# Optimization experiments

Measured on AMD Instinct MI355X. Metric: run time of the kernel, lower is better.

Reference implementation:

```python
import jax, jax.numpy as jnp
import numpy as np

TOP_K = 8          # n_activated_experts
ROUTE_SCALE = 2.5  # route_scale


def setup_inputs() -> dict:
    key = jax.random.key(0)
    k1, k2, k3 = jax.random.split(key, 3)
    T, D, E = 16384, 7168, 256
    x = jax.random.normal(k1, (T, D), dtype=jnp.float32)
    # nn.Linear weight layout: [out_features, in_features]
    W = jax.random.normal(k2, (E, D), dtype=jnp.float32) * (1.0 / np.sqrt(D))
    bias = jax.random.normal(k3, (E,), dtype=jnp.float32) * 0.01
    return {"x": x, "W": W, "bias": bias}


def reference(x, W, bias):
    # logits: [T, E] = x [T, D] @ W.T [D, E]
    logits = jnp.einsum("td,ed->te", x, W)
    scores = jax.nn.sigmoid(logits)              # original_scores
    biased = scores + bias                       # bias only affects expert selection
    _, indices = jax.lax.top_k(biased, TOP_K)    # [T, K] int32
    weights = jnp.take_along_axis(scores, indices, axis=-1)  # gather unbiased scores
    weights = weights / jnp.sum(weights, axis=-1, keepdims=True)  # sigmoid renorm
    weights = weights * ROUTE_SCALE
    return weights.astype(x.dtype), indices
```

## Files before the change

### kernel.cpp

```cpp
#include <hip/hip_runtime.h>
#include <cmath>

namespace {

typedef _Float16 half8 __attribute__((ext_vector_type(8)));
typedef float f32x4 __attribute__((ext_vector_type(4)));

constexpr int kTokens = 16384;
constexpr int kD      = 7168;
constexpr int kE      = 256;
constexpr int kTopK   = 8;
constexpr float kRouteScale = 2.5f;

constexpr int BM     = 64;
constexpr int BK     = 32;
constexpr int KSTEP  = 128;
constexpr int NT     = kD / BK;
constexpr int NSTEP  = kD / KSTEP;
constexpr float kS  = 4096.0f;
constexpr float kC  = 0.000244140625f;
constexpr size_t kWsTileB = 32768;
constexpr size_t kWsNeed  = (size_t)NT * kWsTileB;

__global__ void wconv_kernel(const float* __restrict__ W, unsigned char* __restrict__ ws)
{
    const int e = blockIdx.x;
    const int t = threadIdx.x;
    const float* src = W + (size_t)e * kD + (size_t)t * 8;
    float v[8];
    *reinterpret_cast<float4*>(v)     = *reinterpret_cast<const float4*>(src);
    *reinterpret_cast<float4*>(v + 4) = *reinterpret_cast<const float4*>(src + 4);
    half8 h, l;
#pragma unroll
    for (int j = 0; j < 8; ++j) {
        _Float16 hh = (_Float16)v[j];
        h[j] = hh;
        l[j] = (_Float16)((v[j] - (float)hh) * kS);
    }
    const int kt = t >> 2;
    const int kg = t & 3;
    const size_t off = (size_t)kt * kWsTileB +
                       (size_t)(((e >> 4) << 6) + (kg << 4) + (e & 15)) * 16;
    *reinterpret_cast<half8*>(ws + off)         = h;
    *reinterpret_cast<half8*>(ws + off + 16384) = l;
}

__global__ __launch_bounds__(1024, 4)
void gate_mfma(const float* __restrict__ x,
               const unsigned char* __restrict__ wst,
               const float* __restrict__ bias,
               float* __restrict__ out)
{
    __shared__ unsigned char lds[65792];

    const int t    = threadIdx.x;
    const int lane = t & 63;
    const int w    = t >> 6;
    const int cg   = w >> 1;
    const int rg   = w & 1;
    const int kk0  = cg & 3;
    const int m0   = blockIdx.x * BM;
    const int l15  = lane & 15;
    const int lg   = lane >> 4;

    const int srow = t >> 4;
    const int skc  = t & 15;
    const unsigned waddr = (unsigned)(((skc >> 2) << 13) + ((srow >> 4) << 10) +
                                      ((skc & 3) << 8) + ((((srow & 15) ^ skc) & 15) << 4));
    const float* xsrc = x + (size_t)(m0 + srow) * kD + (size_t)(skc * 8);

    const unsigned char* wb = wst + (size_t)(cg * 2) * 1024 + (size_t)lane * 16;

    f32x4 acc0[2][2], acc1[2][2], accL[2][2];
#pragma unroll
    for (int i = 0; i < 2; ++i)
#pragma unroll
        for (int j = 0; j < 2; ++j) {
            acc0[i][j] = f32x4{0.f,0.f,0.f,0.f};
            acc1[i][j] = f32x4{0.f,0.f,0.f,0.f};
            accL[i][j] = f32x4{0.f,0.f,0.f,0.f};
        }

    half8 bh[2][2];
    half8 bl[2];

    auto LOADBH = [&](int pp, int kt) {
        const unsigned char* p = wb + (size_t)kt * kWsTileB;
        bh[pp][0] = *reinterpret_cast<const half8*>(p);
        bh[pp][1] = *reinterpret_cast<const half8*>(p + 1024);
    };
    auto LOADBL = [&](int kt) {
        const unsigned char* p = wb + (size_t)kt * kWsTileB + 16384;
        bl[0] = *reinterpret_cast<const half8*>(p);
        bl[1] = *reinterpret_cast<const half8*>(p + 1024);
    };
    auto WRITESTEP = [&](unsigned base, const float4& a, const float4& b) {
        float v[8];
        *reinterpret_cast<float4*>(v)     = a;
        *reinterpret_cast<float4*>(v + 4) = b;
        half8 h0, h1;
#pragma unroll
        for (int j = 0; j < 8; ++j) {
            const _Float16 hh = (_Float16)v[j];
            h0[j] = hh;
            h1[j] = (_Float16)((v[j] - (float)hh) * kS);
        }
        *reinterpret_cast<half8*>(&lds[base + waddr])        = h0;
        *reinterpret_cast<half8*>(&lds[base + waddr + 4096]) = h1;
    };

    {
        float4 a = *reinterpret_cast<const float4*>(xsrc);
        float4 b = *reinterpret_cast<const float4*>(xsrc + 4);
        LOADBH(0, kk0);
        WRITESTEP(0, a, b);
    }
    __syncthreads();

    for (int s = 0; s < NSTEP; ++s) {
        const unsigned bufc = (unsigned)((s & 1) << 15);
        const unsigned bufn = (unsigned)(((s + 1) & 1) << 15);
        const bool pre = (s + 1 < NSTEP);
        float4 nv0{0,0,0,0}, nv1{0,0,0,0};
        if (pre) {
            const float* p = xsrc + (s + 1) * KSTEP;
            nv0 = *reinterpret_cast<const float4*>(p);
            nv1 = *reinterpret_cast<const float4*>(p + 4);
        }

#pragma unroll
        for (int n = 0; n < 4; ++n) {
            const int kk = (kk0 + n) & 3;
            const int kt = s * 4 + kk;
            LOADBL(kt);
            const int kt_next = (n < 3) ? (s * 4 + ((kk0 + n + 1) & 3))
                                        : ((s + 1) * 4 + kk0);
            if (kt_next < NT) LOADBH((n & 1) ^ 1, kt_next);

            half8 xh[2], xm[2];
#pragma unroll
            for (int i = 0; i < 2; ++i) {
                const int rf = rg * 2 + i;
                const unsigned base = bufc + (unsigned)(kk << 13) + (unsigned)(rf << 10) +
                                      (unsigned)(lg << 8) +
                                      (unsigned)((((l15 ^ ((kk << 2) + lg)) & 15) << 4));
                xh[i] = *reinterpret_cast<const half8*>(&lds[base]);
                xm[i] = *reinterpret_cast<const half8*>(&lds[base + 4096]);
            }

            __builtin_amdgcn_s_setprio(1);
#pragma unroll
            for (int i = 0; i < 2; ++i)
#pragma unroll
                for (int j = 0; j < 2; ++j)
                    acc0[i][j] = __builtin_amdgcn_mfma_f32_16x16x32_f16(xh[i], bh[n & 1][j], acc0[i][j], 0, 0, 0);
#pragma unroll
            for (int i = 0; i < 2; ++i)
#pragma unroll
                for (int j = 0; j < 2; ++j)
                    acc1[i][j] = __builtin_amdgcn_mfma_f32_16x16x32_f16(xm[i], bh[n & 1][j], acc1[i][j], 0, 0, 0);
#pragma unroll
            for (int i = 0; i < 2; ++i)
#pragma unroll
                for (int j = 0; j < 2; ++j)
                    acc1[i][j] = __builtin_amdgcn_mfma_f32_16x16x32_f16(xh[i], bl[j], acc1[i][j], 0, 0, 0);
            __builtin_amdgcn_s_setprio(0);
        }

        if (pre) WRITESTEP(bufn, nv0, nv1);

        if (((s + 1) & 7) == 0) {
#pragma unroll
            for (int i = 0; i < 2; ++i)
#pragma unroll
                for (int j = 0; j < 2; ++j) {
                    accL[i][j] += acc0[i][j];
                    acc0[i][j] = f32x4{0.f,0.f,0.f,0.f};
                }
        }
        __syncthreads();
    }

    float (*sc)[257] = reinterpret_cast<float (*)[257]>(lds);
#pragma unroll
    for (int j = 0; j < 2; ++j) {
        const int col  = cg * 32 + j * 16 + l15;
        const float bv = bias[col];
#pragma unroll
        for (int i = 0; i < 2; ++i) {
            f32x4 z = (accL[i][j] + acc0[i][j]) + kC * acc1[i][j];
#pragma unroll
            for (int r = 0; r < 4; ++r) {
                const int row = rg * 32 + i * 16 + lg * 4 + r;
                const float sg = 1.0f / (1.0f + expf(-z[r]));
                sc[row][col] = sg + bv;
            }
        }
    }
    __syncthreads();

    const int rr = t >> 4;
    const int g  = t & 15;

    float cval[kTopK];
    int   cidx[kTopK];

#pragma unroll
    for (int r = 0; r < kTopK; ++r) {
        float best = -INFINITY;
        int   bi   = kE;
        const float* rowp = sc[rr] + g * 16;
#pragma unroll 8
        for (int c = 0; c < 16; ++c) {
            const float v  = rowp[c];
            const int   ci = g * 16 + c;
            if (v > best || (v == best && ci < bi)) { best = v; bi = ci; }
        }
#pragma unroll
        for (int off = 8; off > 0; off >>= 1) {
            const float ov = __shfl_xor(best, off, 16);
            const int   oi = __shfl_xor(bi,   off, 16);
            if (ov > best || (ov == best && oi < bi)) { best = ov; bi = oi; }
        }
        cval[r] = best;
        cidx[r] = bi;
        if ((bi >> 4) == g) sc[rr][bi] = -INFINITY;
    }

    if (g == 0) {
        float uw[kTopK];
        float wsum = 0.0f;
#pragma unroll
        for (int r = 0; r < kTopK; ++r) {
            uw[r] = cval[r] - bias[cidx[r]];
            wsum += uw[r];
        }
        const float scale = kRouteScale / wsum;
        const size_t grow = (size_t)(m0 + rr);
#pragma unroll
        for (int r = 0; r < kTopK; ++r)
            out[grow * kTopK + r] = uw[r] * scale;
#pragma unroll
        for (int r = 0; r < kTopK; ++r)
            out[(size_t)kTokens * kTopK + grow * kTopK + r] = (float)cidx[r];
    }
}

constexpr int FBM = 32;
constexpr int FBK = 32;
constexpr int XS_STRIDE = 36;
constexpr int SC_STRIDE = 260;

__global__ __launch_bounds__(256, 2)
void gate_fused(const float* __restrict__ x,
                const float* __restrict__ W,
                const float* __restrict__ bias,
                float* __restrict__ out)
{
    __shared__ float smem[FBK * XS_STRIDE + FBK * kE];
    float (*xs)[XS_STRIDE] = reinterpret_cast<float (*)[XS_STRIDE]>(smem);
    float (*ws)[kE]        = reinterpret_cast<float (*)[kE]>(smem + FBK * XS_STRIDE);
    float (*sc)[SC_STRIDE] = reinterpret_cast<float (*)[SC_STRIDE]>(smem);

    const int t  = threadIdx.x;
    const int tx = t & 31;
    const int ty = t >> 5;
    const int m0 = blockIdx.x * FBM;
    const int lm = t >> 3;
    const int lc = t & 7;

    float acc[4][8];
    float cmp[4][8];
#pragma unroll
    for (int i = 0; i < 4; ++i)
#pragma unroll
        for (int j = 0; j < 8; ++j) { acc[i][j] = 0.0f; cmp[i][j] = 0.0f; }

    const float* xrow = x + (size_t)(m0 + lm) * kD;
    const float* wrow = W + (size_t)t * kD;

    for (int k0 = 0; k0 < kD; k0 += FBK) {
        float4 xv = *reinterpret_cast<const float4*>(xrow + k0 + 4 * lc);
        float4 wv[8];
#pragma unroll
        for (int i = 0; i < 8; ++i)
            wv[i] = *reinterpret_cast<const float4*>(wrow + k0 + 4 * i);
        __syncthreads();
        xs[4 * lc + 0][lm] = xv.x; xs[4 * lc + 1][lm] = xv.y;
        xs[4 * lc + 2][lm] = xv.z; xs[4 * lc + 3][lm] = xv.w;
#pragma unroll
        for (int i = 0; i < 8; ++i) {
            ws[4 * i + 0][t] = wv[i].x; ws[4 * i + 1][t] = wv[i].y;
            ws[4 * i + 2][t] = wv[i].z; ws[4 * i + 3][t] = wv[i].w;
        }
        __syncthreads();
        float p[4][8];
#pragma unroll
        for (int i = 0; i < 4; ++i)
#pragma unroll
            for (int j = 0; j < 8; ++j) p[i][j] = 0.0f;
#pragma unroll
        for (int k = 0; k < FBK; ++k) {
            float a[4], b[8];
            *reinterpret_cast<float4*>(a)     = *reinterpret_cast<const float4*>(&xs[k][4 * ty]);
            *reinterpret_cast<float4*>(b)     = *reinterpret_cast<const float4*>(&ws[k][4 * tx]);
            *reinterpret_cast<float4*>(b + 4) = *reinterpret_cast<const float4*>(&ws[k][128 + 4 * tx]);
#pragma unroll
            for (int i = 0; i < 4; ++i)
#pragma unroll
                for (int j = 0; j < 8; ++j)
                    p[i][j] = fmaf(a[i], b[j], p[i][j]);
        }
#pragma unroll
        for (int i = 0; i < 4; ++i)
#pragma unroll
            for (int j = 0; j < 8; ++j) {
                const float y = p[i][j] - cmp[i][j];
                const float s = acc[i][j] + y;
                cmp[i][j] = (s - acc[i][j]) - y;
                acc[i][j] = s;
            }
    }
    __syncthreads();
#pragma unroll
    for (int i = 0; i < 4; ++i) {
        const int row = 4 * ty + i;
#pragma unroll
        for (int j = 0; j < 8; ++j) {
            const int col = (j < 4) ? (4 * tx + j) : (128 + 4 * tx + (j - 4));
            const float s = 1.0f / (1.0f + expf(-acc[i][j]));
            sc[row][col] = s + bias[col];
        }
    }
    __syncthreads();
    const int rr = t >> 3;
    const int g  = t & 7;
    float cval[kTopK];
    int   cidx[kTopK];
#pragma unroll
    for (int r = 0; r < kTopK; ++r) {
        float best = -INFINITY;
        int   bi   = kE;
        const float* rowp = sc[rr] + g * 32;
#pragma unroll 8
        for (int c = 0; c < 32; ++c) {
            const float v  = rowp[c];
            const int   ci = g * 32 + c;
            if (v > best || (v == best && ci < bi)) { best = v; bi = ci; }
        }
#pragma unroll
        for (int off = 4; off > 0; off >>= 1) {
            const float ov = __shfl_xor(best, off, 8);
            const int   oi = __shfl_xor(bi,   off, 8);
            if (ov > best || (ov == best && oi < bi)) { best = ov; bi = oi; }
        }
        cval[r] = best; cidx[r] = bi;
        if ((bi >> 5) == g) sc[rr][bi] = -INFINITY;
        __syncthreads();
    }
    if (g == 0) {
        float uw[kTopK];
        float wsum = 0.0f;
#pragma unroll
        for (int r = 0; r < kTopK; ++r) { uw[r] = cval[r] - bias[cidx[r]]; wsum += uw[r]; }
        const float scale = kRouteScale / wsum;
        const size_t grow = (size_t)(m0 + rr);
#pragma unroll
        for (int r = 0; r < kTopK; ++r) out[grow * kTopK + r] = uw[r] * scale;
#pragma unroll
        for (int r = 0; r < kTopK; ++r)
            out[(size_t)kTokens * kTopK + grow * kTopK + r] = (float)cidx[r];
    }
}

}

extern "C" void kernel_launch(void* const* d_in, const int* in_sizes, int n_in,
                              void* d_out, int out_size, void* d_ws, size_t ws_size,
                              hipStream_t stream)
{
    const float* x    = (const float*)d_in[0];
    const float* W    = (const float*)d_in[1];
    const float* bias = (const float*)d_in[2];
    float* out = (float*)d_out;

    if (ws_size >= kWsNeed) {
        unsigned char* ws = (unsigned char*)d_ws;
        hipLaunchKernelGGL(wconv_kernel, dim3(kE), dim3(kD / 8), 0, stream, W, ws);
        hipLaunchKernelGGL(gate_mfma, dim3(kTokens / BM), dim3(1024), 0, stream, x, ws, bias, out);
    } else {
        hipLaunchKernelGGL(gate_fused, dim3(kTokens / FBM), dim3(256), 0, stream, x, W, bias, out);
    }
}
```

Baseline: 264.9 us.

## Halve block to 512 threads with 2x4 per-wave MFMA tiles and register double-buffering

```diff
diff --git a/kernel.cpp b/kernel.cpp
--- a/kernel.cpp
+++ b/kernel.cpp
@@ -45,7 +45,7 @@
     *reinterpret_cast<half8*>(ws + off + 16384) = l;
 }
 
-__global__ __launch_bounds__(1024, 4)
+__global__ __launch_bounds__(512, 2)
 void gate_mfma(const float* __restrict__ x,
                const unsigned char* __restrict__ wst,
                const float* __restrict__ bias,
@@ -56,135 +56,138 @@
     const int t    = threadIdx.x;
     const int lane = t & 63;
     const int w    = t >> 6;
-    const int cg   = w >> 1;
-    const int rg   = w & 1;
-    const int kk0  = cg & 3;
+    const int cg   = w & 3;
+    const int rg   = w >> 2;
     const int m0   = blockIdx.x * BM;
     const int l15  = lane & 15;
     const int lg   = lane >> 4;
 
-    const int srow = t >> 4;
-    const int skc  = t & 15;
-    const unsigned waddr = (unsigned)(((skc >> 2) << 13) + ((srow >> 4) << 10) +
-                                      ((skc & 3) << 8) + ((((srow & 15) ^ skc) & 15) << 4));
-    const float* xsrc = x + (size_t)(m0 + srow) * kD + (size_t)(skc * 8);
-
-    const unsigned char* wb = wst + (size_t)(cg * 2) * 1024 + (size_t)lane * 16;
-
-    f32x4 acc0[2][2], acc1[2][2], accL[2][2];
+    const int srow = t >> 3;
+    const int sc8  = t & 7;
+    const unsigned wbase = (unsigned)(((sc8 >> 1) << 13) + ((srow >> 4) << 10) +
+                                      ((sc8 & 1) << 9) + ((srow & 15) << 4));
+    const float* xsrc = x + (size_t)(m0 + srow) * kD + (size_t)(sc8 * 16);
+
+    const unsigned arb = (unsigned)((rg * 2) * 1024 + lane * 16);
+
+    const unsigned char* wb = wst + (size_t)(cg * 4) * 1024 + (size_t)lane * 16;
+
+    f32x4 acc0[2][4], acc1[2][4], accL[2][4];
 #pragma unroll
     for (int i = 0; i < 2; ++i)
 #pragma unroll
-        for (int j = 0; j < 2; ++j) {
+        for (int j = 0; j < 4; ++j) {
             acc0[i][j] = f32x4{0.f,0.f,0.f,0.f};
             acc1[i][j] = f32x4{0.f,0.f,0.f,0.f};
             accL[i][j] = f32x4{0.f,0.f,0.f,0.f};
         }
 
-    half8 bh[2][2];
-    half8 bl[2];
-
-    auto LOADBH = [&](int pp, int kt) {
-        const unsigned char* p = wb + (size_t)kt * kWsTileB;
-        bh[pp][0] = *reinterpret_cast<const half8*>(p);
-        bh[pp][1] = *reinterpret_cast<const half8*>(p + 1024);
+    half8 ax[2][2][2];
+    half8 bx[2][2][4];
+
+    auto LOADB = [&](int p, int kt) {
+        const unsigned char* q = wb + (size_t)kt * kWsTileB;
+#pragma unroll
+        for (int j = 0; j < 4; ++j) {
+            bx[p][0][j] = *reinterpret_cast<const half8*>(q + j * 1024);
+            bx[p][1][j] = *reinterpret_cast<const half8*>(q + j * 1024 + 16384);
+        }
     };
-    auto LOADBL = [&](int kt) {
-        const unsigned char* p = wb + (size_t)kt * kWsTileB + 16384;
-        bl[0] = *reinterpret_cast<const half8*>(p);
-        bl[1] = *reinterpret_cast<const half8*>(p + 1024);
+    auto LDA = [&](int p, unsigned buf, int kk) {
+        const unsigned base = buf + (unsigned)(kk << 13) + arb;
+#pragma unroll
+        for (int i = 0; i < 2; ++i) {
+            ax[p][0][i] = *reinterpret_cast<const half8*>(&lds[base + i * 1024]);
+            ax[p][1][i] = *reinterpret_cast<const half8*>(&lds[base + i * 1024 + 4096]);
+        }
     };
-    auto WRITESTEP = [&](unsigned base, const float4& a, const float4& b) {
-        float v[8];
-        *reinterpret_cast<float4*>(v)     = a;
-        *reinterpret_cast<float4*>(v + 4) = b;
-        half8 h0, h1;
+    auto WRITESTEP = [&](unsigned buf, const float4* q) {
+        float v[16];
+#pragma unroll
+        for (int p = 0; p < 4; ++p) *reinterpret_cast<float4*>(v + 4 * p) = q[p];
+        half8 h0a, h0b, h1a, h1b;
 #pragma unroll
         for (int j = 0; j < 8; ++j) {
-            const _Float16 hh = (_Float16)v[j];
-            h0[j] = hh;
-            h1[j] = (_Float16)((v[j] - (float)hh) * kS);
-        }
-        *reinterpret_cast<half8*>(&lds[base + waddr])        = h0;
-        *reinterpret_cast<half8*>(&lds[base + waddr + 4096]) = h1;
+            { const float vv = v[j];     const _Float16 hh = (_Float16)vv;
+              h0a[j] = hh; h1a[j] = (_Float16)((vv - (float)hh) * kS); }
+            { const float vv = v[j + 8]; const _Float16 hh = (_Float16)vv;
+              h0b[j] = hh; h1b[j] = (_Float16)((vv - (float)hh) * kS); }
+        }
+        const unsigned base = buf + wbase;
+        *reinterpret_cast<half8*>(&lds[base])               = h0a;
+        *reinterpret_cast<half8*>(&lds[base + 256])         = h0b;
+        *reinterpret_cast<half8*>(&lds[base + 4096])        = h1a;
+        *reinterpret_cast<half8*>(&lds[base + 4096 + 256])  = h1b;
     };
+    auto CLUSTER = [&](int p) {
+#pragma unroll
+        for (int j = 0; j < 4; ++j)
+#pragma unroll
+            for (int i = 0; i < 2; ++i)
+                acc0[i][j] = __builtin_amdgcn_mfma_f32_16x16x32_f16(ax[p][0][i], bx[p][0][j], acc0[i][j], 0, 0, 0);
+#pragma unroll
+        for (int j = 0; j < 4; ++j)
+#pragma unroll
+            for (int i = 0; i < 2; ++i)
+                acc1[i][j] = __builtin_amdgcn_mfma_f32_16x16x32_f16(ax[p][1][i], bx[p][0][j], acc1[i][j], 0, 0, 0);
+#pragma unroll
+        for (int j = 0; j < 4; ++j)
+#pragma unroll
+            for (int i = 0; i < 2; ++i)
+                acc1[i][j] = __builtin_amdgcn_mfma_f32_16x16x32_f16(ax[p][0][i], bx[p][1][j], acc1[i][j], 0, 0, 0);
+    };
 
     {
-        float4 a = *reinterpret_cast<const float4*>(xsrc);
-        float4 b = *reinterpret_cast<const float4*>(xsrc + 4);
-        LOADBH(0, kk0);
-        WRITESTEP(0, a, b);
+        float4 q[4];
+#pragma unroll
+        for (int p = 0; p < 4; ++p)
+            q[p] = *reinterpret_cast<const float4*>(xsrc + 4 * p);
+        LOADB(0, 0);
+        WRITESTEP(0, q);
     }
     __syncthreads();
+    LDA(0, 0, 0);
 
     for (int s = 0; s < NSTEP; ++s) {
         const unsigned bufc = (unsigned)((s & 1) << 15);
-        const unsigned bufn = (unsigned)(((s + 1) & 1) << 15);
+        const unsigned bufn = bufc ^ 32768u;
         const bool pre = (s + 1 < NSTEP);
-        float4 nv0{0,0,0,0}, nv1{0,0,0,0};
+        float4 q[4];
         if (pre) {
-            const float* p = xsrc + (s + 1) * KSTEP;
-            nv0 = *reinterpret_cast<const float4*>(p);
-            nv1 = *reinterpret_cast<const float4*>(p + 4);
-        }
-
-#pragma unroll
-        for (int n = 0; n < 4; ++n) {
-            const int kk = (kk0 + n) & 3;
+            const float* p = xsrc + (size_t)(s + 1) * KSTEP;
+#pragma unroll
+            for (int i = 0; i < 4; ++i)
+                q[i] = *reinterpret_cast<const float4*>(p + 4 * i);
+        }
+
+#pragma unroll
+        for (int kk = 0; kk < 4; ++kk) {
+            const int p  = kk & 1;
             const int kt = s * 4 + kk;
-            LOADBL(kt);
-            const int kt_next = (n < 3) ? (s * 4 + ((kk0 + n + 1) & 3))
-                                        : ((s + 1) * 4 + kk0);
-            if (kt_next < NT) LOADBH((n & 1) ^ 1, kt_next);
-
-            half8 xh[2], xm[2];
-#pragma unroll
-            for (int i = 0; i < 2; ++i) {
-                const int rf = rg * 2 + i;
-                const unsigned base = bufc + (unsigned)(kk << 13) + (unsigned)(rf << 10) +
-                                      (unsigned)(lg << 8) +
-                                      (unsigned)((((l15 ^ ((kk << 2) + lg)) & 15) << 4));
-                xh[i] = *reinterpret_cast<const half8*>(&lds[base]);
-                xm[i] = *reinterpret_cast<const half8*>(&lds[base + 4096]);
-            }
-
-            __builtin_amdgcn_s_setprio(1);
+            if (kk < 3) LDA(p ^ 1, bufc, kk + 1);
+            if (kt + 1 < NT) LOADB(p ^ 1, kt + 1);
+            CLUSTER(p);
+        }
+
+        if (pre) WRITESTEP(bufn, q);
+
+        if ((s & 3) == 3) {
 #pragma unroll
             for (int i = 0; i < 2; ++i)
 #pragma unroll
-                for (int j = 0; j < 2; ++j)
-                    acc0[i][j] = __builtin_amdgcn_mfma_f32_16x16x32_f16(xh[i], bh[n & 1][j], acc0[i][j], 0, 0, 0);
-#pragma unroll
-            for (int i = 0; i < 2; ++i)
-#pragma unroll
-                for (int j = 0; j < 2; ++j)
-                    acc1[i][j] = __builtin_amdgcn_mfma_f32_16x16x32_f16(xm[i], bh[n & 1][j], acc1[i][j], 0, 0, 0);
-#pragma unroll
-            for (int i = 0; i < 2; ++i)
-#pragma unroll
-                for (int j = 0; j < 2; ++j)
-                    acc1[i][j] = __builtin_amdgcn_mfma_f32_16x16x32_f16(xh[i], bl[j], acc1[i][j], 0, 0, 0);
-            __builtin_amdgcn_s_setprio(0);
-        }
-
-        if (pre) WRITESTEP(bufn, nv0, nv1);
-
-        if (((s + 1) & 7) == 0) {
-#pragma unroll
-            for (int i = 0; i < 2; ++i)
-#pragma unroll
-                for (int j = 0; j < 2; ++j) {
+                for (int j = 0; j < 4; ++j) {
                     accL[i][j] += acc0[i][j];
                     acc0[i][j] = f32x4{0.f,0.f,0.f,0.f};
                 }
         }
         __syncthreads();
+        if (pre) LDA(0, bufn, 0);
     }
 
     float (*sc)[257] = reinterpret_cast<float (*)[257]>(lds);
 #pragma unroll
-    for (int j = 0; j < 2; ++j) {
-        const int col  = cg * 32 + j * 16 + l15;
+    for (int j = 0; j < 4; ++j) {
+        const int col  = cg * 64 + j * 16 + l15;
         const float bv = bias[col];
 #pragma unroll
         for (int i = 0; i < 2; ++i) {
@@ -199,8 +202,8 @@
     }
     __syncthreads();
 
-    const int rr = t >> 4;
-    const int g  = t & 15;
+    const int rr = t >> 3;
+    const int g  = t & 7;
 
     float cval[kTopK];
     int   cidx[kTopK];
@@ -209,22 +212,22 @@
     for (int r = 0; r < kTopK; ++r) {
         float best = -INFINITY;
         int   bi   = kE;
-        const float* rowp = sc[rr] + g * 16;
+        const float* rowp = sc[rr] + g * 32;
 #pragma unroll 8
-        for (int c = 0; c < 16; ++c) {
+        for (int c = 0; c < 32; ++c) {
             const float v  = rowp[c];
-            const int   ci = g * 16 + c;
+            const int   ci = g * 32 + c;
             if (v > best || (v == best && ci < bi)) { best = v; bi = ci; }
         }
 #pragma unroll
-        for (int off = 8; off > 0; off >>= 1) {
-            const float ov = __shfl_xor(best, off, 16);
-            const int   oi = __shfl_xor(bi,   off, 16);
+        for (int off = 4; off > 0; off >>= 1) {
+            const float ov = __shfl_xor(best, off, 8);
+            const int   oi = __shfl_xor(bi,   off, 8);
             if (ov > best || (ov == best && oi < bi)) { best = ov; bi = oi; }
         }
         cval[r] = best;
         cidx[r] = bi;
-        if ((bi >> 4) == g) sc[rr][bi] = -INFINITY;
+        if ((bi >> 5) == g) sc[rr][bi] = -INFINITY;
     }
 
     if (g == 0) {
@@ -387,7 +390,7 @@
     if (ws_size >= kWsNeed) {
         unsigned char* ws = (unsigned char*)d_ws;
         hipLaunchKernelGGL(wconv_kernel, dim3(kE), dim3(kD / 8), 0, stream, W, ws);
-        hipLaunchKernelGGL(gate_mfma, dim3(kTokens / BM), dim3(1024), 0, stream, x, ws, bias, out);
+        hipLaunchKernelGGL(gate_mfma, dim3(kTokens / BM), dim3(512), 0, stream, x, ws, bias, out);
     } else {
         hipLaunchKernelGGL(gate_fused, dim3(kTokens / FBM), dim3(256), 0, stream, x, W, bias, out);
     }
```

Result: slower. 283.0 us (+6.8%).
